# Kernel optimization log

Hardware: AMD Instinct MI355X
Metric: run time of the kernel (lower is better)

The kernel has to match this reference:

```python
import jax, jax.numpy as jnp
import numpy as np

B, T, I, H = 512, 2048, 13, 13


def setup_inputs() -> dict:
    key = jax.random.key(0)
    ks = jax.random.split(key, 7)
    s_in = 1.0 / np.sqrt(H)
    return {
        "x": jax.random.normal(ks[0], (B, T, I), dtype=jnp.float32),
        "W_ih": jax.random.uniform(ks[1], (4 * H, I), jnp.float32, -s_in, s_in),
        "W_hh": jax.random.uniform(ks[2], (4 * H, H), jnp.float32, -s_in, s_in),
        "b_ih": jax.random.uniform(ks[3], (4 * H,), jnp.float32, -s_in, s_in),
        "b_hh": jax.random.uniform(ks[4], (4 * H,), jnp.float32, -s_in, s_in),
        "fc_w": jax.random.uniform(ks[5], (1, H), jnp.float32, -s_in, s_in),
        "fc_b": jax.random.uniform(ks[6], (1,), jnp.float32, -s_in, s_in),
    }


def _lstm(x, W_ih, W_hh, b_ih, b_hh):
    # Precompute input-to-gate projections for all timesteps: [B, T, 4H]
    xg = jnp.einsum("bti,gi->btg", x, W_ih) + b_ih + b_hh
    xg = jnp.swapaxes(xg, 0, 1)  # [T, B, 4H] for scan
    h0 = jnp.zeros((x.shape[0], H), x.dtype)
    c0 = jnp.zeros((x.shape[0], H), x.dtype)

    def step(carry, xg_t):
        h, c = carry
        gates = xg_t + h @ W_hh.T  # [B, 4H]
        i_g, f_g, g_g, o_g = jnp.split(gates, 4, axis=-1)  # PyTorch order i,f,g,o
        i_g = jax.nn.sigmoid(i_g)
        f_g = jax.nn.sigmoid(f_g)
        g_g = jnp.tanh(g_g)
        o_g = jax.nn.sigmoid(o_g)
        c_new = f_g * c + i_g * g_g
        h_new = o_g * jnp.tanh(c_new)
        return (h_new, c_new), h_new

    _, hs = jax.lax.scan(step, (h0, c0), xg)  # hs: [T, B, H]
    return jnp.swapaxes(hs, 0, 1)  # [B, T, H]


def reference(x, W_ih, W_hh, b_ih, b_hh, fc_w, fc_b):
    out = _lstm(x, W_ih, W_hh, b_ih, b_hh)  # [B, T, H]
    out = jnp.einsum("bth,oh->bto", out, fc_w) + fc_b  # [B, T, 1]
    return jax.nn.sigmoid(out)
```

## Files before the change

### kernel.cpp

```cpp
#include <hip/hip_runtime.h>
#include <hip/hip_fp16.h>

#define BB 512
#define TT 2048

typedef _Float16 half2v __attribute__((ext_vector_type(2)));

__device__ __forceinline__ float fexp2(float x){ return __builtin_amdgcn_exp2f(x); }
__device__ __forceinline__ float frcp(float x){ return __builtin_amdgcn_rcpf(x); }
__device__ __forceinline__ float sigm(float x){ return frcp(1.f + fexp2(-1.4426950408889634f*x)); }
__device__ __forceinline__ float tanhfast(float x){ return 1.f - 2.f*frcp(1.f + fexp2(2.8853900817779268f*x)); }

#define QB(v, ctrl) __int_as_float(__builtin_amdgcn_mov_dpp(__float_as_int(v), (ctrl), 0xF, 0xF, true))
#define RL(v, l)    __builtin_amdgcn_readlane((v), (l))

__global__ __launch_bounds__(256) void k_xg3(const float* __restrict__ x,
                                             const float* __restrict__ Wih,
                                             const float* __restrict__ bih,
                                             const float* __restrict__ bhh,
                                             const float* __restrict__ fcb,
                                             unsigned* __restrict__ xg_u)
{
  __shared__ float    xs[13*256];
  __shared__ unsigned ot[32*212];
  const int tid = threadIdx.x;
  const int b   = blockIdx.x >> 3;
  const int t0  = (blockIdx.x & 7) << 8;

  const float* xsrc = x + ((size_t)b*TT + t0)*13;
  #pragma unroll
  for (int it=0; it<13; ++it) xs[tid + it*256] = xsrc[tid + it*256];
  __syncthreads();

  float xv[13];
  #pragma unroll
  for (int k=0;k<13;k++) xv[k] = xs[tid*13+k];

  const int tgl = tid >> 3, u = tid & 7;
  unsigned short* otp = (unsigned short*)ot;
  #pragma unroll 2
  for (int g=0; g<52; ++g){
    float acc = bih[g] + bhh[g];
    #pragma unroll
    for (int k=0;k<13;k++) acc = fmaf(Wih[g*13+k], xv[k], acc);
    const float sc = (g>=26 && g<39) ? -2.8853900817779268f : -1.4426950408889634f;
    otp[tgl*424 + g*8 + u] = __half_as_ushort(__float2half(acc*sc));
  }
  otp[tgl*424 + 52*8 + u] =
      __half_as_ushort(__float2half(-1.4426950408889634f * fcb[0]));
  __syncthreads();

  unsigned* dst = xg_u + (size_t)b*(256*212) + (size_t)(blockIdx.x & 7)*(32*212);
  #pragma unroll
  for (int it=0; it<27; ++it){
    int i2 = tid + it*256;
    if (i2 < 32*212) dst[i2] = ot[i2];
  }
}

__global__ __launch_bounds__(64, 1) void k_rec7(const float* __restrict__ Whh,
                                                const float* __restrict__ fcw,
                                                const float* __restrict__ fcb,
                                                const unsigned short* __restrict__ xg,
                                                float* __restrict__ out)
{
  const int lane = threadIdx.x;
  const int b    = blockIdx.x;
  const int q    = lane & 3;
  const int j    = lane >> 2;
  const int jc   = (j < 13) ? j : 12;
  const int e    = (lane == 52) ? 52 : q*13 + jc;

  const float kq = (q==2) ? -2.8853900817779268f : -1.4426950408889634f;
  const float gm = (q==2) ? -5.7707801635558536f : 1.f;
  const float ga = (q==2) ?  2.8853900817779268f : 0.f;
  const float fcbias = -1.4426950408889634f * fcb[0];

  const float* wsrc = (lane == 52) ? fcw : (Whh + e*13);
  float w[13];
  #pragma unroll
  for (int k=0;k<13;k++) w[k] = wsrc[k]*kq;

  const char* gbase = (const char*)xg + (size_t)b*(256*848) + (size_t)e*16;

  float h = 0.f, c_ = 0.f;
  float hb0=0,hb1=0,hb2=0,hb3=0,hb4=0,hb5=0,hb6=0,hb7=0,hb8=0,hb9=0,hb10=0,hb11=0,hb12=0;

  float p0=0,p1=0,p2=0,p3=0,p4=0,p5=0,p6=0,p7=0;
  float* op = out + (size_t)b*TT;
  bool first = true;

#define CAPTURE(gv_, u_) do {                                                 \
    if ((u_)==1) p0=(gv_); else if ((u_)==2) p1=(gv_);                        \
    else if ((u_)==3) p2=(gv_); else if ((u_)==4) p3=(gv_);                   \
    else if ((u_)==5) p4=(gv_); else if ((u_)==6) p5=(gv_);                   \
    else if ((u_)==7) p6=(gv_);                                               \
    else { p7=(gv_);                                                          \
      if (!first){                                                            \
        if (lane == 52){                                                      \
          float4* o4 = (float4*)op;                                           \
          o4[0] = make_float4(p0,p1,p2,p3);                                   \
          o4[1] = make_float4(p4,p5,p6,p7);                                   \
        }                                                                     \
        op += 8;                                                              \
      }                                                                       \
      first = false;                                                          \
    }                                                                         \
  } while(0)

#define STEP(xv_, u_) do {                                                    \
    float dA = fmaf(w[0], hb0, (xv_));                                        \
    dA = fmaf(w[1], hb1, dA);                                                 \
    dA = fmaf(w[2], hb2, dA);                                                 \
    dA = fmaf(w[3], hb3, dA);                                                 \
    dA = fmaf(w[4], hb4, dA);                                                 \
    float dB = w[5]*hb5;                                                      \
    dB = fmaf(w[6], hb6, dB);                                                 \
    dB = fmaf(w[7], hb7, dB);                                                 \
    dB = fmaf(w[8], hb8, dB);                                                 \
    float dC = w[9]*hb9;                                                      \
    dC = fmaf(w[10], hb10, dC);                                               \
    dC = fmaf(w[11], hb11, dC);                                               \
    dC = fmaf(w[12], hb12, dC);                                               \
    float s  = (dB + dC) + dA;                                                \
    float r  = frcp(1.f + fexp2(s));                                          \
    float g  = fmaf(gm, r, ga);                                               \
    CAPTURE(g, u_);                                                           \
    float ggb = QB(g, 0xAA);                                                  \
    float gfb = QB(g, 0x55);                                                  \
    float gob = QB(g, 0xFF);                                                  \
    float go2 = gob + gob;                                                    \
    c_ = fmaf(gfb, c_, g*ggb);                                                \
    float r2 = frcp(1.f + fexp2(c_));                                         \
    h = fmaf(go2, r2, -gob);                                                  \
    int hv_ = __float_as_int(h);                                              \
    hb0  = __int_as_float(RL(hv_, 0));                                        \
    hb1  = __int_as_float(RL(hv_, 4));                                        \
    hb2  = __int_as_float(RL(hv_, 8));                                        \
    hb3  = __int_as_float(RL(hv_, 12));                                       \
    hb4  = __int_as_float(RL(hv_, 16));                                       \
    hb5  = __int_as_float(RL(hv_, 20));                                       \
    hb6  = __int_as_float(RL(hv_, 24));                                       \
    hb7  = __int_as_float(RL(hv_, 28));                                       \
    hb8  = __int_as_float(RL(hv_, 32));                                       \
    hb9  = __int_as_float(RL(hv_, 36));                                       \
    hb10 = __int_as_float(RL(hv_, 40));                                       \
    hb11 = __int_as_float(RL(hv_, 44));                                       \
    hb12 = __int_as_float(RL(hv_, 48));                                       \
  } while(0)

#define XLO(w_) (float)(__builtin_bit_cast(half2v, (w_)).x)
#define XHI(w_) (float)(__builtin_bit_cast(half2v, (w_)).y)

#define STEP8(Q) do {                                                         \
    STEP(XLO(Q.x), 0); STEP(XHI(Q.x), 1);                                     \
    STEP(XLO(Q.y), 2); STEP(XHI(Q.y), 3);                                     \
    STEP(XLO(Q.z), 4); STEP(XHI(Q.z), 5);                                     \
    STEP(XLO(Q.w), 6); STEP(XHI(Q.w), 7);                                     \
  } while(0)

  uint4 q0 = *(const uint4*)(gbase);
  uint4 q1 = *(const uint4*)(gbase + 848);
  uint4 q2 = *(const uint4*)(gbase + 2*848);
  uint4 q3 = *(const uint4*)(gbase + 3*848);

  for (int i=0; i<63; ++i){
    const char* pn = gbase + (size_t)(4*i+4)*848;
    uint4 c0 = q0; q0 = *(const uint4*)(pn);
    STEP8(c0);
    uint4 c1 = q1; q1 = *(const uint4*)(pn + 848);
    STEP8(c1);
    uint4 c2 = q2; q2 = *(const uint4*)(pn + 2*848);
    STEP8(c2);
    uint4 c3 = q3; q3 = *(const uint4*)(pn + 3*848);
    STEP8(c3);
  }
  STEP8(q0); STEP8(q1); STEP8(q2); STEP8(q3);

  {
    float s = fcbias;
    s = fmaf(w[0],  hb0,  s);
    s = fmaf(w[1],  hb1,  s);
    s = fmaf(w[2],  hb2,  s);
    s = fmaf(w[3],  hb3,  s);
    s = fmaf(w[4],  hb4,  s);
    s = fmaf(w[5],  hb5,  s);
    s = fmaf(w[6],  hb6,  s);
    s = fmaf(w[7],  hb7,  s);
    s = fmaf(w[8],  hb8,  s);
    s = fmaf(w[9],  hb9,  s);
    s = fmaf(w[10], hb10, s);
    s = fmaf(w[11], hb11, s);
    s = fmaf(w[12], hb12, s);
    float r = frcp(1.f + fexp2(s));
    if (lane == 52){
      float4* o4 = (float4*)op;
      o4[0] = make_float4(p0,p1,p2,p3);
      o4[1] = make_float4(p4,p5,p6,r);
    }
  }

#undef STEP8
#undef STEP
#undef CAPTURE
#undef XLO
#undef XHI
}

__global__ __launch_bounds__(64) void k_rec_fb(
    const float* __restrict__ x,   const float* __restrict__ Whh,
    const float* __restrict__ Wih, const float* __restrict__ bih, const float* __restrict__ bhh,
    const float* __restrict__ fcw, const float* __restrict__ fcb,
    float* __restrict__ out)
{
  const int lane = threadIdx.x;
  const int c    = lane >> 4;
  const int j    = lane & 15;
  const int b    = blockIdx.x*4 + c;
  const bool act = (j < 13);
  const int jj   = act ? j : 0;

  float whh[4][13], wih[4][13], bias[4];
  #pragma unroll
  for (int q=0;q<4;q++){
    #pragma unroll
    for (int k=0;k<13;k++){
      float w1 = Whh[(q*13+jj)*13 + k];
      float w2 = Wih[(q*13+jj)*13 + k];
      whh[q][k] = act ? w1 : 0.f;
      wih[q][k] = act ? w2 : 0.f;
    }
    bias[q] = bih[q*13+jj] + bhh[q*13+jj];
  }
  const float fcwj = act ? fcw[jj] : 0.f;
  const float fcb0 = fcb[0];

  const float* xpf = x + (size_t)b*(TT*13) + jj;
  float* op = out + (size_t)b*TT;

  float h = 0.f, cs = 0.f;
  float xsc = *xpf;

  for (int t=0; t<TT; ++t){
    float xscn = 0.f;
    if (t+1 < TT) { xpf += 13; xscn = *xpf; }

    float hb[13], xb[13];
    {
      int hbits = __float_as_int(h);
      int xbits = __float_as_int(xsc);
      #define HB(k) hb[k] = __int_as_float(__builtin_amdgcn_ds_swizzle(hbits, ((k)<<5)|0x10)); \
                    xb[k] = __int_as_float(__builtin_amdgcn_ds_swizzle(xbits, ((k)<<5)|0x10));
      HB(0) HB(1) HB(2) HB(3) HB(4) HB(5) HB(6) HB(7) HB(8) HB(9) HB(10) HB(11) HB(12)
      #undef HB
    }
    float a0 = bias[0], a1 = bias[1], a2 = bias[2], a3 = bias[3];
    #pragma unroll
    for (int k=0;k<13;k++){
      float xk = xb[k], hk = hb[k];
      a0 += wih[0][k]*xk + whh[0][k]*hk;
      a1 += wih[1][k]*xk + whh[1][k]*hk;
      a2 += wih[2][k]*xk + whh[2][k]*hk;
      a3 += wih[3][k]*xk + whh[3][k]*hk;
    }
    float ig = sigm(a0), fg = sigm(a1), gg = tanhfast(a2), og = sigm(a3);
    cs = fg*cs + ig*gg;
    h  = og * tanhfast(cs);

    float p = act ? fcwj*h : 0.f;
    #define RED(m) p += __int_as_float(__builtin_amdgcn_ds_swizzle(__float_as_int(p), ((m)<<10)|0x1F));
    RED(1) RED(2) RED(4) RED(8)
    #undef RED
    if (j == 0) op[t] = sigm(p + fcb0);
    xsc = xscn;
  }
}

extern "C" void kernel_launch(void* const* d_in, const int* in_sizes, int n_in,
                              void* d_out, int out_size, void* d_ws, size_t ws_size,
                              hipStream_t stream)
{
  const float* x   = (const float*)d_in[0];
  const float* Wih = (const float*)d_in[1];
  const float* Whh = (const float*)d_in[2];
  const float* bih = (const float*)d_in[3];
  const float* bhh = (const float*)d_in[4];
  const float* fcw = (const float*)d_in[5];
  const float* fcb = (const float*)d_in[6];
  float* out = (float*)d_out;

  const size_t XG_BYTES = (size_t)BB*256*848;

  if (ws_size >= XG_BYTES){
    unsigned* xg = (unsigned*)d_ws;
    k_xg3<<<dim3(BB*8), dim3(256), 0, stream>>>(x, Wih, bih, bhh, fcb, xg);
    k_rec7<<<dim3(BB), dim3(64), 0, stream>>>(Whh, fcw, fcb,
                                              (const unsigned short*)xg, out);
  } else {
    k_rec_fb<<<dim3(BB/4), dim3(64), 0, stream>>>(x, Whh, Wih, bih, bhh, fcw, fcb, out);
  }
}
```

Baseline: 323.9 us.

## Fuse input projection and recurrence into one kernel per batch row

Merges the input-projection kernel and the recurrent kernel into a single 256-thread block per batch element. The block first computes all eight time chunks of fp16 gate preactivations into workspace, then one wavefront runs the serial recurrence. This removes a kernel launch and the device-wide boundary between the two phases, so each row can start its recurrence as soon as its own projection is done. In exchange the projection now runs on only 512 blocks, serialised over eight chunks, and three of the four waves sit idle during the long recurrence.

```diff
diff --git a/kernel.cpp b/kernel.cpp
--- a/kernel.cpp
+++ b/kernel.cpp
@@ -14,58 +14,61 @@
 #define QB(v, ctrl) __int_as_float(__builtin_amdgcn_mov_dpp(__float_as_int(v), (ctrl), 0xF, 0xF, true))
 #define RL(v, l)    __builtin_amdgcn_readlane((v), (l))
 
-__global__ __launch_bounds__(256) void k_xg3(const float* __restrict__ x,
-                                             const float* __restrict__ Wih,
-                                             const float* __restrict__ bih,
-                                             const float* __restrict__ bhh,
-                                             const float* __restrict__ fcb,
-                                             unsigned* __restrict__ xg_u)
+__global__ __launch_bounds__(256, 1) void k_fused(const float* __restrict__ x,
+                                                  const float* __restrict__ Wih,
+                                                  const float* __restrict__ Whh,
+                                                  const float* __restrict__ bih,
+                                                  const float* __restrict__ bhh,
+                                                  const float* __restrict__ fcw,
+                                                  const float* __restrict__ fcb,
+                                                  unsigned short* __restrict__ xg,
+                                                  float* __restrict__ out)
 {
   __shared__ float    xs[13*256];
   __shared__ unsigned ot[32*212];
   const int tid = threadIdx.x;
-  const int b   = blockIdx.x >> 3;
-  const int t0  = (blockIdx.x & 7) << 8;
-
-  const float* xsrc = x + ((size_t)b*TT + t0)*13;
-  #pragma unroll
-  for (int it=0; it<13; ++it) xs[tid + it*256] = xsrc[tid + it*256];
+  const int b   = blockIdx.x;
+
+  char* xgb = (char*)xg + (size_t)b*(256*848);
+  const float fcb0 = fcb[0];
+
+  for (int c=0; c<8; ++c){
+    const float* xsrc = x + ((size_t)b*TT + (c<<8))*13;
+    #pragma unroll
+    for (int it=0; it<13; ++it) xs[tid + it*256] = xsrc[tid + it*256];
+    __syncthreads();
+
+    float xv[13];
+    #pragma unroll
+    for (int k=0;k<13;k++) xv[k] = xs[tid*13+k];
+
+    const int tgl = tid >> 3, u = tid & 7;
+    unsigned short* otp = (unsigned short*)ot;
+    #pragma unroll 2
+    for (int g=0; g<52; ++g){
+      float acc = bih[g] + bhh[g];
+      #pragma unroll
+      for (int k=0;k<13;k++) acc = fmaf(Wih[g*13+k], xv[k], acc);
+      const float sc = (g>=26 && g<39) ? -2.8853900817779268f : -1.4426950408889634f;
+      otp[tgl*424 + g*8 + u] = __half_as_ushort(__float2half(acc*sc));
+    }
+    otp[tgl*424 + 52*8 + u] =
+        __half_as_ushort(__float2half(-1.4426950408889634f * fcb0));
+    __syncthreads();
+
+    unsigned* dst = (unsigned*)(xgb + (size_t)c*(32*848));
+    #pragma unroll
+    for (int it=0; it<27; ++it){
+      int i2 = tid + it*256;
+      if (i2 < 32*212) dst[i2] = ot[i2];
+    }
+    __syncthreads();
+  }
   __syncthreads();
 
-  float xv[13];
-  #pragma unroll
-  for (int k=0;k<13;k++) xv[k] = xs[tid*13+k];
-
-  const int tgl = tid >> 3, u = tid & 7;
-  unsigned short* otp = (unsigned short*)ot;
-  #pragma unroll 2
-  for (int g=0; g<52; ++g){
-    float acc = bih[g] + bhh[g];
-    #pragma unroll
-    for (int k=0;k<13;k++) acc = fmaf(Wih[g*13+k], xv[k], acc);
-    const float sc = (g>=26 && g<39) ? -2.8853900817779268f : -1.4426950408889634f;
-    otp[tgl*424 + g*8 + u] = __half_as_ushort(__float2half(acc*sc));
-  }
-  otp[tgl*424 + 52*8 + u] =
-      __half_as_ushort(__float2half(-1.4426950408889634f * fcb[0]));
-  __syncthreads();
-
-  unsigned* dst = xg_u + (size_t)b*(256*212) + (size_t)(blockIdx.x & 7)*(32*212);
-  #pragma unroll
-  for (int it=0; it<27; ++it){
-    int i2 = tid + it*256;
-    if (i2 < 32*212) dst[i2] = ot[i2];
-  }
-}
-
-__global__ __launch_bounds__(64, 1) void k_rec7(const float* __restrict__ Whh,
-                                                const float* __restrict__ fcw,
-                                                const float* __restrict__ fcb,
-                                                const unsigned short* __restrict__ xg,
-                                                float* __restrict__ out)
-{
-  const int lane = threadIdx.x;
-  const int b    = blockIdx.x;
+  if (tid >= 64) return;
+
+  const int lane = tid;
   const int q    = lane & 3;
   const int j    = lane >> 2;
   const int jc   = (j < 13) ? j : 12;
@@ -74,14 +77,14 @@
   const float kq = (q==2) ? -2.8853900817779268f : -1.4426950408889634f;
   const float gm = (q==2) ? -5.7707801635558536f : 1.f;
   const float ga = (q==2) ?  2.8853900817779268f : 0.f;
-  const float fcbias = -1.4426950408889634f * fcb[0];
+  const float fcbias = -1.4426950408889634f * fcb0;
 
   const float* wsrc = (lane == 52) ? fcw : (Whh + e*13);
   float w[13];
   #pragma unroll
   for (int k=0;k<13;k++) w[k] = wsrc[k]*kq;
 
-  const char* gbase = (const char*)xg + (size_t)b*(256*848) + (size_t)e*16;
+  const char* gbase = (const char*)xgb + (size_t)e*16;
 
   float h = 0.f, c_ = 0.f;
   float hb0=0,hb1=0,hb2=0,hb3=0,hb4=0,hb5=0,hb6=0,hb7=0,hb8=0,hb9=0,hb10=0,hb11=0,hb12=0;
@@ -292,10 +295,8 @@
   const size_t XG_BYTES = (size_t)BB*256*848;
 
   if (ws_size >= XG_BYTES){
-    unsigned* xg = (unsigned*)d_ws;
-    k_xg3<<<dim3(BB*8), dim3(256), 0, stream>>>(x, Wih, bih, bhh, fcb, xg);
-    k_rec7<<<dim3(BB), dim3(64), 0, stream>>>(Whh, fcw, fcb,
-                                              (const unsigned short*)xg, out);
+    k_fused<<<dim3(BB), dim3(256), 0, stream>>>(x, Wih, Whh, bih, bhh, fcw, fcb,
+                                                (unsigned short*)d_ws, out);
   } else {
     k_rec_fb<<<dim3(BB/4), dim3(64), 0, stream>>>(x, Whh, Wih, bih, bhh, fcw, fcb, out);
   }
```

Result: slower. 343.1 us (+5.9%).

## Interleave two independent batch recurrences per wavefront to hide latency

Applied to the files above, without the earlier changes.

Each wavefront now runs the LSTM recurrence for two batch rows at once, interleaving their steps so the serial dependency chains (exp/rcp, DPP, readlane) of one row can overlap with the other's. Grid size is halved to 256 blocks, and prefetch depth changes to a rolling two-group buffer per row. This adds instruction-level parallelism within a wave but halves wave count on a large GPU and increases register pressure.

```diff
diff --git a/kernel.cpp b/kernel.cpp
--- a/kernel.cpp
+++ b/kernel.cpp
@@ -58,14 +58,15 @@
   }
 }
 
-__global__ __launch_bounds__(64, 1) void k_rec7(const float* __restrict__ Whh,
-                                                const float* __restrict__ fcw,
-                                                const float* __restrict__ fcb,
-                                                const unsigned short* __restrict__ xg,
-                                                float* __restrict__ out)
+__global__ __launch_bounds__(64, 1) void k_rec11(const float* __restrict__ Whh,
+                                                 const float* __restrict__ fcw,
+                                                 const float* __restrict__ fcb,
+                                                 const unsigned short* __restrict__ xg,
+                                                 float* __restrict__ out)
 {
   const int lane = threadIdx.x;
-  const int b    = blockIdx.x;
+  const int bA   = blockIdx.x*2;
+  const int bB   = bA + 1;
   const int q    = lane & 3;
   const int j    = lane >> 2;
   const int jc   = (j < 13) ? j : 12;
@@ -81,128 +82,131 @@
   #pragma unroll
   for (int k=0;k<13;k++) w[k] = wsrc[k]*kq;
 
-  const char* gbase = (const char*)xg + (size_t)b*(256*848) + (size_t)e*16;
-
-  float h = 0.f, c_ = 0.f;
-  float hb0=0,hb1=0,hb2=0,hb3=0,hb4=0,hb5=0,hb6=0,hb7=0,hb8=0,hb9=0,hb10=0,hb11=0,hb12=0;
-
-  float p0=0,p1=0,p2=0,p3=0,p4=0,p5=0,p6=0,p7=0;
-  float* op = out + (size_t)b*TT;
-  bool first = true;
-
-#define CAPTURE(gv_, u_) do {                                                 \
-    if ((u_)==1) p0=(gv_); else if ((u_)==2) p1=(gv_);                        \
-    else if ((u_)==3) p2=(gv_); else if ((u_)==4) p3=(gv_);                   \
-    else if ((u_)==5) p4=(gv_); else if ((u_)==6) p5=(gv_);                   \
-    else if ((u_)==7) p6=(gv_);                                               \
-    else { p7=(gv_);                                                          \
-      if (!first){                                                            \
+  const char* gbaseA = (const char*)xg + (size_t)bA*(256*848) + (size_t)e*16;
+  const char* gbaseB = (const char*)xg + (size_t)bB*(256*848) + (size_t)e*16;
+
+  float hA=0.f, c_A=0.f, hB=0.f, c_B=0.f;
+  float hb0A=0,hb1A=0,hb2A=0,hb3A=0,hb4A=0,hb5A=0,hb6A=0,hb7A=0,hb8A=0,hb9A=0,hb10A=0,hb11A=0,hb12A=0;
+  float hb0B=0,hb1B=0,hb2B=0,hb3B=0,hb4B=0,hb5B=0,hb6B=0,hb7B=0,hb8B=0,hb9B=0,hb10B=0,hb11B=0,hb12B=0;
+  float p0A=0,p1A=0,p2A=0,p3A=0,p4A=0,p5A=0,p6A=0,p7A=0;
+  float p0B=0,p1B=0,p2B=0,p3B=0,p4B=0,p5B=0,p6B=0,p7B=0;
+  float* opA = out + (size_t)bA*TT;
+  float* opB = out + (size_t)bB*TT;
+  bool firstA = true, firstB = true;
+
+#define CAPT(S, gv_, u_) do {                                                 \
+    if ((u_)==1) p0##S=(gv_); else if ((u_)==2) p1##S=(gv_);                  \
+    else if ((u_)==3) p2##S=(gv_); else if ((u_)==4) p3##S=(gv_);             \
+    else if ((u_)==5) p4##S=(gv_); else if ((u_)==6) p5##S=(gv_);             \
+    else if ((u_)==7) p6##S=(gv_);                                            \
+    else { p7##S=(gv_);                                                       \
+      if (!first##S){                                                         \
         if (lane == 52){                                                      \
-          float4* o4 = (float4*)op;                                           \
-          o4[0] = make_float4(p0,p1,p2,p3);                                   \
-          o4[1] = make_float4(p4,p5,p6,p7);                                   \
+          float4* o4 = (float4*)op##S;                                        \
+          o4[0] = make_float4(p0##S,p1##S,p2##S,p3##S);                       \
+          o4[1] = make_float4(p4##S,p5##S,p6##S,p7##S);                       \
         }                                                                     \
-        op += 8;                                                              \
+        op##S += 8;                                                           \
       }                                                                       \
-      first = false;                                                          \
+      first##S = false;                                                       \
     }                                                                         \
   } while(0)
 
-#define STEP(xv_, u_) do {                                                    \
-    float dA = fmaf(w[0], hb0, (xv_));                                        \
-    dA = fmaf(w[1], hb1, dA);                                                 \
-    dA = fmaf(w[2], hb2, dA);                                                 \
-    dA = fmaf(w[3], hb3, dA);                                                 \
-    dA = fmaf(w[4], hb4, dA);                                                 \
-    float dB = w[5]*hb5;                                                      \
-    dB = fmaf(w[6], hb6, dB);                                                 \
-    dB = fmaf(w[7], hb7, dB);                                                 \
-    dB = fmaf(w[8], hb8, dB);                                                 \
-    float dC = w[9]*hb9;                                                      \
-    dC = fmaf(w[10], hb10, dC);                                               \
-    dC = fmaf(w[11], hb11, dC);                                               \
-    dC = fmaf(w[12], hb12, dC);                                               \
-    float s  = (dB + dC) + dA;                                                \
-    float r  = frcp(1.f + fexp2(s));                                          \
-    float g  = fmaf(gm, r, ga);                                               \
-    CAPTURE(g, u_);                                                           \
-    float ggb = QB(g, 0xAA);                                                  \
-    float gfb = QB(g, 0x55);                                                  \
-    float gob = QB(g, 0xFF);                                                  \
-    float go2 = gob + gob;                                                    \
-    c_ = fmaf(gfb, c_, g*ggb);                                                \
-    float r2 = frcp(1.f + fexp2(c_));                                         \
-    h = fmaf(go2, r2, -gob);                                                  \
-    int hv_ = __float_as_int(h);                                              \
-    hb0  = __int_as_float(RL(hv_, 0));                                        \
-    hb1  = __int_as_float(RL(hv_, 4));                                        \
-    hb2  = __int_as_float(RL(hv_, 8));                                        \
-    hb3  = __int_as_float(RL(hv_, 12));                                       \
-    hb4  = __int_as_float(RL(hv_, 16));                                       \
-    hb5  = __int_as_float(RL(hv_, 20));                                       \
-    hb6  = __int_as_float(RL(hv_, 24));                                       \
-    hb7  = __int_as_float(RL(hv_, 28));                                       \
-    hb8  = __int_as_float(RL(hv_, 32));                                       \
-    hb9  = __int_as_float(RL(hv_, 36));                                       \
-    hb10 = __int_as_float(RL(hv_, 40));                                       \
-    hb11 = __int_as_float(RL(hv_, 44));                                       \
-    hb12 = __int_as_float(RL(hv_, 48));                                       \
+#define STEPC(S, xv_, u_) do {                                                \
+    float dA_ = fmaf(w[0], hb0##S, (xv_));                                    \
+    dA_ = fmaf(w[1], hb1##S, dA_);                                            \
+    dA_ = fmaf(w[2], hb2##S, dA_);                                            \
+    dA_ = fmaf(w[3], hb3##S, dA_);                                            \
+    dA_ = fmaf(w[4], hb4##S, dA_);                                            \
+    float dB_ = w[5]*hb5##S;                                                  \
+    dB_ = fmaf(w[6], hb6##S, dB_);                                            \
+    dB_ = fmaf(w[7], hb7##S, dB_);                                            \
+    dB_ = fmaf(w[8], hb8##S, dB_);                                            \
+    float dC_ = w[9]*hb9##S;                                                  \
+    dC_ = fmaf(w[10], hb10##S, dC_);                                          \
+    dC_ = fmaf(w[11], hb11##S, dC_);                                          \
+    dC_ = fmaf(w[12], hb12##S, dC_);                                          \
+    float s_  = (dB_ + dC_) + dA_;                                            \
+    float r_  = frcp(1.f + fexp2(s_));                                        \
+    float g_  = fmaf(gm, r_, ga);                                             \
+    CAPT(S, g_, u_);                                                          \
+    float ggb_ = QB(g_, 0xAA);                                                \
+    float gfb_ = QB(g_, 0x55);                                                \
+    float gob_ = QB(g_, 0xFF);                                                \
+    float go2_ = gob_ + gob_;                                                 \
+    c_##S = fmaf(gfb_, c_##S, g_*ggb_);                                       \
+    float r2_ = frcp(1.f + fexp2(c_##S));                                     \
+    h##S = fmaf(go2_, r2_, -gob_);                                            \
+    int hv_ = __float_as_int(h##S);                                           \
+    hb0##S  = __int_as_float(RL(hv_, 0));                                     \
+    hb1##S  = __int_as_float(RL(hv_, 4));                                     \
+    hb2##S  = __int_as_float(RL(hv_, 8));                                     \
+    hb3##S  = __int_as_float(RL(hv_, 12));                                    \
+    hb4##S  = __int_as_float(RL(hv_, 16));                                    \
+    hb5##S  = __int_as_float(RL(hv_, 20));                                    \
+    hb6##S  = __int_as_float(RL(hv_, 24));                                    \
+    hb7##S  = __int_as_float(RL(hv_, 28));                                    \
+    hb8##S  = __int_as_float(RL(hv_, 32));                                    \
+    hb9##S  = __int_as_float(RL(hv_, 36));                                    \
+    hb10##S = __int_as_float(RL(hv_, 40));                                    \
+    hb11##S = __int_as_float(RL(hv_, 44));                                    \
+    hb12##S = __int_as_float(RL(hv_, 48));                                    \
   } while(0)
 
 #define XLO(w_) (float)(__builtin_bit_cast(half2v, (w_)).x)
 #define XHI(w_) (float)(__builtin_bit_cast(half2v, (w_)).y)
 
-#define STEP8(Q) do {                                                         \
-    STEP(XLO(Q.x), 0); STEP(XHI(Q.x), 1);                                     \
-    STEP(XLO(Q.y), 2); STEP(XHI(Q.y), 3);                                     \
-    STEP(XLO(Q.z), 4); STEP(XHI(Q.z), 5);                                     \
-    STEP(XLO(Q.w), 6); STEP(XHI(Q.w), 7);                                     \
-  } while(0)
-
-  uint4 q0 = *(const uint4*)(gbase);
-  uint4 q1 = *(const uint4*)(gbase + 848);
-  uint4 q2 = *(const uint4*)(gbase + 2*848);
-  uint4 q3 = *(const uint4*)(gbase + 3*848);
-
-  for (int i=0; i<63; ++i){
-    const char* pn = gbase + (size_t)(4*i+4)*848;
-    uint4 c0 = q0; q0 = *(const uint4*)(pn);
-    STEP8(c0);
-    uint4 c1 = q1; q1 = *(const uint4*)(pn + 848);
-    STEP8(c1);
-    uint4 c2 = q2; q2 = *(const uint4*)(pn + 2*848);
-    STEP8(c2);
-    uint4 c3 = q3; q3 = *(const uint4*)(pn + 3*848);
-    STEP8(c3);
-  }
-  STEP8(q0); STEP8(q1); STEP8(q2); STEP8(q3);
+  uint4 qA0 = *(const uint4*)(gbaseA);
+  uint4 qA1 = *(const uint4*)(gbaseA + 848);
+  uint4 qB0 = *(const uint4*)(gbaseB);
+  uint4 qB1 = *(const uint4*)(gbaseB + 848);
+
+  for (int tg=0; tg<256; ++tg){
+    const int pf = (tg+2 < 256) ? tg+2 : 255;
+    uint4 cA = qA0; qA0 = qA1; qA1 = *(const uint4*)(gbaseA + (size_t)pf*848);
+    uint4 cB = qB0; qB0 = qB1; qB1 = *(const uint4*)(gbaseB + (size_t)pf*848);
+
+    STEPC(A, XLO(cA.x), 0); STEPC(B, XLO(cB.x), 0);
+    STEPC(A, XHI(cA.x), 1); STEPC(B, XHI(cB.x), 1);
+    STEPC(A, XLO(cA.y), 2); STEPC(B, XLO(cB.y), 2);
+    STEPC(A, XHI(cA.y), 3); STEPC(B, XHI(cB.y), 3);
+    STEPC(A, XLO(cA.z), 4); STEPC(B, XLO(cB.z), 4);
+    STEPC(A, XHI(cA.z), 5); STEPC(B, XHI(cB.z), 5);
+    STEPC(A, XLO(cA.w), 6); STEPC(B, XLO(cB.w), 6);
+    STEPC(A, XHI(cA.w), 7); STEPC(B, XHI(cB.w), 7);
+  }
 
   {
     float s = fcbias;
-    s = fmaf(w[0],  hb0,  s);
-    s = fmaf(w[1],  hb1,  s);
-    s = fmaf(w[2],  hb2,  s);
-    s = fmaf(w[3],  hb3,  s);
-    s = fmaf(w[4],  hb4,  s);
-    s = fmaf(w[5],  hb5,  s);
-    s = fmaf(w[6],  hb6,  s);
-    s = fmaf(w[7],  hb7,  s);
-    s = fmaf(w[8],  hb8,  s);
-    s = fmaf(w[9],  hb9,  s);
-    s = fmaf(w[10], hb10, s);
-    s = fmaf(w[11], hb11, s);
-    s = fmaf(w[12], hb12, s);
-    float r = frcp(1.f + fexp2(s));
+    s = fmaf(w[0],  hb0A,  s);  s = fmaf(w[1],  hb1A,  s);
+    s = fmaf(w[2],  hb2A,  s);  s = fmaf(w[3],  hb3A,  s);
+    s = fmaf(w[4],  hb4A,  s);  s = fmaf(w[5],  hb5A,  s);
+    s = fmaf(w[6],  hb6A,  s);  s = fmaf(w[7],  hb7A,  s);
+    s = fmaf(w[8],  hb8A,  s);  s = fmaf(w[9],  hb9A,  s);
+    s = fmaf(w[10], hb10A, s);  s = fmaf(w[11], hb11A, s);
+    s = fmaf(w[12], hb12A, s);
+    float rA = frcp(1.f + fexp2(s));
+    float t = fcbias;
+    t = fmaf(w[0],  hb0B,  t);  t = fmaf(w[1],  hb1B,  t);
+    t = fmaf(w[2],  hb2B,  t);  t = fmaf(w[3],  hb3B,  t);
+    t = fmaf(w[4],  hb4B,  t);  t = fmaf(w[5],  hb5B,  t);
+    t = fmaf(w[6],  hb6B,  t);  t = fmaf(w[7],  hb7B,  t);
+    t = fmaf(w[8],  hb8B,  t);  t = fmaf(w[9],  hb9B,  t);
+    t = fmaf(w[10], hb10B, t);  t = fmaf(w[11], hb11B, t);
+    t = fmaf(w[12], hb12B, t);
+    float rB = frcp(1.f + fexp2(t));
     if (lane == 52){
-      float4* o4 = (float4*)op;
-      o4[0] = make_float4(p0,p1,p2,p3);
-      o4[1] = make_float4(p4,p5,p6,r);
+      float4* o4 = (float4*)opA;
+      o4[0] = make_float4(p0A,p1A,p2A,p3A);
+      o4[1] = make_float4(p4A,p5A,p6A,rA);
+      float4* o5 = (float4*)opB;
+      o5[0] = make_float4(p0B,p1B,p2B,p3B);
+      o5[1] = make_float4(p4B,p5B,p6B,rB);
     }
   }
 
-#undef STEP8
-#undef STEP
-#undef CAPTURE
+#undef STEPC
+#undef CAPT
 #undef XLO
 #undef XHI
 }
@@ -294,8 +298,8 @@
   if (ws_size >= XG_BYTES){
     unsigned* xg = (unsigned*)d_ws;
     k_xg3<<<dim3(BB*8), dim3(256), 0, stream>>>(x, Wih, bih, bhh, fcb, xg);
-    k_rec7<<<dim3(BB), dim3(64), 0, stream>>>(Whh, fcw, fcb,
-                                              (const unsigned short*)xg, out);
+    k_rec11<<<dim3(BB/2), dim3(64), 0, stream>>>(Whh, fcw, fcb,
+                                                 (const unsigned short*)xg, out);
   } else {
     k_rec_fb<<<dim3(BB/4), dim3(64), 0, stream>>>(x, Whh, Wih, bih, bhh, fcw, fcb, out);
   }
```

Result: slower. 531.0 us (+64.0%).
